# Performance work log

Hardware: AMD Instinct MI355X
Metric: run time of the kernel (lower is better)

Reference implementation:

```python
import jax, jax.numpy as jnp
import numpy as np

NUM_USERS = 100000
NUM_ITEMS = 50000
NUM_NODES = NUM_USERS + NUM_ITEMS
EMB = 64
NUM_EDGES = 2000000
BATCH = 16384


def setup_inputs() -> dict:
    key = jax.random.key(0)
    ks = jax.random.split(key, 9)

    def xavier(k, shape):
        fan_in, fan_out = shape[-2], shape[-1]
        lim = float(np.sqrt(6.0 / (fan_in + fan_out)))
        return jax.random.uniform(k, shape, jnp.float32, -lim, lim)

    user_table = xavier(ks[0], (NUM_USERS, EMB))
    item_table = xavier(ks[1], (NUM_ITEMS, EMB))
    # gat1: in=64, heads=4, out=64 -> W1 [64, 256]; a1 [4, 128]
    W1 = xavier(ks[2], (EMB, EMB * 4))
    a1 = xavier(ks[3], (4, 2 * EMB))
    # gat2: in=256, heads=1, out=64 -> W2 [256, 64]; a2 [1, 128]
    W2 = xavier(ks[4], (EMB * 4, EMB))
    a2 = xavier(ks[5], (1, 2 * EMB))

    edge_index = jax.random.randint(ks[6], (2, NUM_EDGES), 0, NUM_NODES, dtype=jnp.int32)
    user_ids = jax.random.randint(ks[7], (BATCH,), 0, NUM_USERS, dtype=jnp.int32)
    item_ids = jax.random.randint(ks[8], (BATCH,), 0, NUM_ITEMS, dtype=jnp.int32)
    return {
        "user_table": user_table, "item_table": item_table,
        "W1": W1, "a1": a1, "W2": W2, "a2": a2,
        "edge_index": edge_index, "user_ids": user_ids, "item_ids": item_ids,
    }


def gat_layer(x, W, a, num_heads, out_features, src, dst, concat):
    n = x.shape[0]
    h = (x @ W).reshape(n, num_heads, out_features)          # [N,H,F]
    # attention score: (cat(h_src,h_dst) * a).sum(-1) == h_src.a_l + h_dst.a_r
    a_l, a_r = a[:, :out_features], a[:, out_features:]
    e_src = jnp.einsum('nhf,hf->nh', h, a_l)                 # [N,H]
    e_dst = jnp.einsum('nhf,hf->nh', h, a_r)
    att = e_src[src] + e_dst[dst]                            # [E,H]
    att = jnp.where(att > 0, att, 0.2 * att)                 # LeakyReLU(0.2)
    att = jnp.exp(att - jnp.max(att))                        # global max, as in torch code
    att_sum = jax.ops.segment_sum(att, dst, num_segments=n)  # [N,H]
    att = att / (att_sum[dst] + 1e-8)
    msg = att[:, :, None] * h[src]                           # [E,H,F]
    out = jax.ops.segment_sum(msg, dst, num_segments=n)      # [N,H,F]
    return out.reshape(n, -1) if concat else out.mean(axis=1)


def reference(user_table, item_table, W1, a1, W2, a2, edge_index, user_ids, item_ids):
    src, dst = edge_index[0], edge_index[1]
    all_emb = jnp.concatenate([user_table, item_table], axis=0)  # [N,64]
    h = gat_layer(all_emb, W1, a1, 4, EMB, src, dst, concat=True)  # [N,256]
    h = jax.nn.elu(h)
    h = gat_layer(h, W2, a2, 1, EMB, src, dst, concat=False)       # [N,64]
    h = h + all_emb
    user_emb = h[:NUM_USERS]
    item_emb = h[NUM_USERS:]
    return jnp.sum(user_emb[user_ids] * item_emb[item_ids], axis=1)
```

## Files before the change

kernel.cpp:

```cpp
#include <hip/hip_runtime.h>
#include <cstdint>
#include <cstddef>

#define NUM_USERS 100000
#define NUM_ITEMS 50000
#define NUM_NODES 150000
#define NUM_EDGES 2000000
#define BATCH 16384
#define BSHIFT 8
#define NBUCK ((NUM_NODES + 255) >> BSHIFT)
#define PA_EDGES 8192
#define PA_BLOCKS ((NUM_EDGES + PA_EDGES - 1) / PA_EDGES)
#define NNPAD 150016
#define TBLK (NNPAD / 64)

typedef _Float16 hf8 __attribute__((ext_vector_type(8)));
typedef _Float16 hf4 __attribute__((ext_vector_type(4)));
typedef float fx4 __attribute__((ext_vector_type(4)));

__global__ void flag_kernel(const int* __restrict__ uid, const int* __restrict__ iid,
                            int* __restrict__ nodelist, int* __restrict__ bcnt) {
  int i = blockIdx.x * blockDim.x + threadIdx.x;
  if (i < NBUCK) bcnt[i] = 0;
  if (i < BATCH) {
    nodelist[2 * i] = uid[i];
    nodelist[2 * i + 1] = NUM_USERS + iid[i];
  }
}

__global__ __launch_bounds__(256) void bhist_kernel(const int* __restrict__ dst,
                                                    int* __restrict__ bcnt) {
  __shared__ int bh[NBUCK];
  int t = threadIdx.x;
  for (int u = t; u < NBUCK; u += 256) bh[u] = 0;
  __syncthreads();
  int base = blockIdx.x * PA_EDGES;
#pragma unroll
  for (int u = 0; u < PA_EDGES / 256; ++u) {
    int e = base + u * 256 + t;
    if (e < NUM_EDGES) atomicAdd(&bh[dst[e] >> BSHIFT], 1);
  }
  __syncthreads();
  for (int u = t; u < NBUCK; u += 256) {
    int v = bh[u];
    if (v) atomicAdd(&bcnt[u], v);
  }
}

__global__ void bscan_kernel(const int* __restrict__ bcnt, int* __restrict__ bbase,
                             int* __restrict__ bcursor, int* __restrict__ offsets) {
  __shared__ int sh[1024];
  int t = threadIdx.x;
  int v = (t < NBUCK) ? bcnt[t] : 0;
  sh[t] = v;
  __syncthreads();
  for (int off = 1; off < 1024; off <<= 1) {
    int x = (t >= off) ? sh[t - off] : 0;
    __syncthreads();
    sh[t] += x;
    __syncthreads();
  }
  if (t < NBUCK) {
    bbase[t] = sh[t] - v;
    bcursor[t] = sh[t] - v;
  }
  if (t == NBUCK - 1) {
    bbase[NBUCK] = sh[t];
    offsets[NUM_NODES] = sh[t];
  }
}

__global__ __launch_bounds__(256) void bpart_kernel(const int* __restrict__ src,
                                                    const int* __restrict__ dst,
                                                    int* __restrict__ bcursor,
                                                    int2* __restrict__ ebuf) {
  __shared__ int lcnt[NBUCK];
  __shared__ int lbase[NBUCK];
  int t = threadIdx.x;
  for (int u = t; u < NBUCK; u += 256) lcnt[u] = 0;
  __syncthreads();
  int base = blockIdx.x * PA_EDGES;
#pragma unroll
  for (int u = 0; u < PA_EDGES / 256; ++u) {
    int e = base + u * 256 + t;
    if (e < NUM_EDGES) atomicAdd(&lcnt[dst[e] >> BSHIFT], 1);
  }
  __syncthreads();
  for (int u = t; u < NBUCK; u += 256) {
    int v = lcnt[u];
    lbase[u] = v ? atomicAdd(&bcursor[u], v) : 0;
    lcnt[u] = 0;
  }
  __syncthreads();
#pragma unroll
  for (int u = 0; u < PA_EDGES / 256; ++u) {
    int e = base + u * 256 + t;
    if (e < NUM_EDGES) {
      int d = dst[e];
      int b = d >> BSHIFT;
      int p = lbase[b] + atomicAdd(&lcnt[b], 1);
      ebuf[p] = make_int2(src[e], d);
    }
  }
}

__global__ __launch_bounds__(256) void bcsr_kernel(const int2* __restrict__ ebuf,
                                                   const int* __restrict__ bbase,
                                                   int* __restrict__ offsets,
                                                   int* __restrict__ srcs) {
  __shared__ int ncnt[256];
  __shared__ int sh[256];
  __shared__ int lcur[256];
  int b = blockIdx.x;
  int t = threadIdx.x;
  int node0 = b << BSHIFT;
  int ebeg = bbase[b], eend = bbase[b + 1];
  ncnt[t] = 0;
  __syncthreads();
  for (int i = ebeg + t; i < eend; i += 256)
    atomicAdd(&ncnt[ebuf[i].y - node0], 1);
  __syncthreads();
  int v = ncnt[t];
  sh[t] = v;
  __syncthreads();
  for (int off = 1; off < 256; off <<= 1) {
    int x = (t >= off) ? sh[t - off] : 0;
    __syncthreads();
    sh[t] += x;
    __syncthreads();
  }
  int excl = ebeg + sh[t] - v;
  if (node0 + t < NUM_NODES) offsets[node0 + t] = excl;
  lcur[t] = excl;
  __syncthreads();
  for (int i = ebeg + t; i < eend; i += 256) {
    int2 ed = ebuf[i];
    int p = atomicAdd(&lcur[ed.y - node0], 1);
    srcs[p] = ed.x;
  }
}

__global__ void proj1_kernel(const float* __restrict__ W1, const float* __restrict__ a1,
                             float* __restrict__ w1a, float* __restrict__ w1b) {
  int t = threadIdx.x;
  int h = t >> 6, k = t & 63;
  float sa = 0.f, sb = 0.f;
  for (int f = 0; f < 64; ++f) {
    float w = W1[(size_t)k * 256 + h * 64 + f];
    sa += w * a1[h * 128 + f];
    sb += w * a1[h * 128 + 64 + f];
  }
  w1a[h * 64 + k] = sa;
  w1b[h * 64 + k] = sb;
}

__global__ __launch_bounds__(256) void e1_kernel(
    const float* __restrict__ ut, const float* __restrict__ it,
    const float* __restrict__ w1a, const float* __restrict__ w1b,
    float* __restrict__ e1s, float* __restrict__ e1d) {
  int wid = threadIdx.x >> 6, lane = threadIdx.x & 63;
  int node = blockIdx.x * 4 + wid;
  if (node >= NUM_NODES) return;
  const float* x = (node < NUM_USERS) ? ut + (size_t)node * 64
                                      : it + (size_t)(node - NUM_USERS) * 64;
  float xv = x[lane];
#pragma unroll
  for (int h = 0; h < 4; ++h) {
    float ps = xv * w1a[h * 64 + lane];
    float pd = xv * w1b[h * 64 + lane];
#pragma unroll
    for (int off = 32; off; off >>= 1) {
      ps += __shfl_xor(ps, off, 64);
      pd += __shfl_xor(pd, off, 64);
    }
    if (lane == 0) {
      e1s[(size_t)node * 4 + h] = ps;
      e1d[(size_t)node * 4 + h] = pd;
    }
  }
}

__device__ __forceinline__ const float* row_ptr(int s, const float* __restrict__ ut,
                                                const float* __restrict__ it) {
  return (s < NUM_USERS) ? ut + (size_t)s * 64 : it + (size_t)(s - NUM_USERS) * 64;
}

__device__ __forceinline__ float lrexp(float x) {
  x = x > 0.f ? x : 0.2f * x;
  return __expf(x);
}

__device__ __forceinline__ float wnorm(float w) {
  float sum = w;
#pragma unroll
  for (int off = 32; off; off >>= 1) sum += __shfl_xor(sum, off, 64);
  return w * (1.f / (sum + 1e-8f));
}

__device__ __forceinline__ void fold4(float4& a) {
#pragma unroll
  for (int off = 16; off <= 32; off <<= 1) {
    a.x += __shfl_xor(a.x, off, 64);
    a.y += __shfl_xor(a.y, off, 64);
    a.z += __shfl_xor(a.z, off, 64);
    a.w += __shfl_xor(a.w, off, 64);
  }
}

__device__ __forceinline__ float elu(float x) {
  return x > 0.f ? x : (__expf(x) - 1.f);
}

__device__ __forceinline__ void split4(float4 o, hf4& hv, hf4& lv) {
  float a0 = o.x * 256.f, a1 = o.y * 256.f, a2 = o.z * 256.f, a3 = o.w * 256.f;
  _Float16 h0 = (_Float16)a0, h1 = (_Float16)a1;
  _Float16 h2 = (_Float16)a2, h3 = (_Float16)a3;
  hv[0] = h0; hv[1] = h1; hv[2] = h2; hv[3] = h3;
  lv[0] = (_Float16)(a0 - (float)h0);
  lv[1] = (_Float16)(a1 - (float)h1);
  lv[2] = (_Float16)(a2 - (float)h2);
  lv[3] = (_Float16)(a3 - (float)h3);
}

__device__ __forceinline__ void splitstore(_Float16* __restrict__ hi,
                                           _Float16* __restrict__ lo,
                                           size_t idx, float v) {
  v *= 256.f;
  _Float16 h = (_Float16)v;
  hi[idx] = h;
  lo[idx] = (_Float16)(v - (float)h);
}

__global__ __launch_bounds__(256) void aggX4_kernel(
    const int* __restrict__ offsets, const int* __restrict__ srcs,
    const float* __restrict__ e1s, const float* __restrict__ e1d,
    const float* __restrict__ ut, const float* __restrict__ it,
    _Float16* __restrict__ aXhi, _Float16* __restrict__ aXlo) {
  int wid = threadIdx.x >> 6, lane = threadIdx.x & 63;
  int node = blockIdx.x * 4 + wid;
  if (node >= NNPAD) return;
  if (node >= NUM_NODES) {
    *(float2*)(aXhi + (size_t)node * 256 + lane * 4) = make_float2(0.f, 0.f);
    *(float2*)(aXlo + (size_t)node * 256 + lane * 4) = make_float2(0.f, 0.f);
    return;
  }
  int beg = offsets[node], end = offsets[node + 1];
  int deg = end - beg;

  float edv0 = e1d[(size_t)node * 4 + 0];
  float edv1 = e1d[(size_t)node * 4 + 1];
  float edv2 = e1d[(size_t)node * 4 + 2];
  float edv3 = e1d[(size_t)node * 4 + 3];

  if (deg <= 64) {
    int s = 0;
    float w0 = 0.f, w1 = 0.f, w2 = 0.f, w3 = 0.f;
    if (lane < deg) {
      s = srcs[beg + lane];
      float4 ev = *(const float4*)(e1s + (size_t)s * 4);
      w0 = lrexp(ev.x + edv0);
      w1 = lrexp(ev.y + edv1);
      w2 = lrexp(ev.z + edv2);
      w3 = lrexp(ev.w + edv3);
    }
    w0 = wnorm(w0);
    w1 = wnorm(w1);
    w2 = wnorm(w2);
    w3 = wnorm(w3);

    const int g = lane >> 4, fl = lane & 15;
    float4 acc0 = make_float4(0.f, 0.f, 0.f, 0.f);
    float4 acc1 = acc0, acc2 = acc0, acc3 = acc0;
#pragma unroll 4
    for (int e = 0; e < deg; e += 4) {
      int ei = e + g;
      int sg = __shfl(s, ei, 64);
      float4 xv = *(const float4*)(row_ptr(sg, ut, it) + fl * 4);
      float wg0 = __shfl(w0, ei, 64);
      acc0.x += wg0 * xv.x; acc0.y += wg0 * xv.y;
      acc0.z += wg0 * xv.z; acc0.w += wg0 * xv.w;
      float wg1 = __shfl(w1, ei, 64);
      acc1.x += wg1 * xv.x; acc1.y += wg1 * xv.y;
      acc1.z += wg1 * xv.z; acc1.w += wg1 * xv.w;
      float wg2 = __shfl(w2, ei, 64);
      acc2.x += wg2 * xv.x; acc2.y += wg2 * xv.y;
      acc2.z += wg2 * xv.z; acc2.w += wg2 * xv.w;
      float wg3 = __shfl(w3, ei, 64);
      acc3.x += wg3 * xv.x; acc3.y += wg3 * xv.y;
      acc3.z += wg3 * xv.z; acc3.w += wg3 * xv.w;
    }
    fold4(acc0); fold4(acc1); fold4(acc2); fold4(acc3);

    float4 o = (g == 0) ? acc0 : (g == 1) ? acc1 : (g == 2) ? acc2 : acc3;
    hf4 hv, lv;
    split4(o, hv, lv);
    *(hf4*)(aXhi + (size_t)node * 256 + lane * 4) = hv;
    *(hf4*)(aXlo + (size_t)node * 256 + lane * 4) = lv;
  } else {
    float s0 = 0.f, s1 = 0.f, s2 = 0.f, s3 = 0.f;
    for (int e = beg + lane; e < end; e += 64) {
      int s = srcs[e];
      float4 ev = *(const float4*)(e1s + (size_t)s * 4);
      s0 += lrexp(ev.x + edv0); s1 += lrexp(ev.y + edv1);
      s2 += lrexp(ev.z + edv2); s3 += lrexp(ev.w + edv3);
    }
#pragma unroll
    for (int off = 32; off; off >>= 1) {
      s0 += __shfl_xor(s0, off, 64);
      s1 += __shfl_xor(s1, off, 64);
      s2 += __shfl_xor(s2, off, 64);
      s3 += __shfl_xor(s3, off, 64);
    }
    float i0 = 1.f / (s0 + 1e-8f), i1 = 1.f / (s1 + 1e-8f);
    float i2 = 1.f / (s2 + 1e-8f), i3 = 1.f / (s3 + 1e-8f);
    float a0 = 0.f, a1 = 0.f, a2 = 0.f, a3 = 0.f;
    for (int e = beg; e < end; ++e) {
      int sn = srcs[e];
      float xv = row_ptr(sn, ut, it)[lane];
      float4 ev = *(const float4*)(e1s + (size_t)sn * 4);
      a0 += lrexp(ev.x + edv0) * i0 * xv;
      a1 += lrexp(ev.y + edv1) * i1 * xv;
      a2 += lrexp(ev.z + edv2) * i2 * xv;
      a3 += lrexp(ev.w + edv3) * i3 * xv;
    }
    splitstore(aXhi, aXlo, (size_t)node * 256 + 0 * 64 + lane, a0);
    splitstore(aXhi, aXlo, (size_t)node * 256 + 1 * 64 + lane, a1);
    splitstore(aXhi, aXlo, (size_t)node * 256 + 2 * 64 + lane, a2);
    splitstore(aXhi, aXlo, (size_t)node * 256 + 3 * 64 + lane, a3);
  }
}

__global__ void wprep_kernel(const float* __restrict__ W1, const float* __restrict__ W2,
                             _Float16* __restrict__ w1t_hi, _Float16* __restrict__ w1t_lo,
                             _Float16* __restrict__ w2t_hi, _Float16* __restrict__ w2t_lo) {
  int t = threadIdx.x;
  int h = t >> 6, a = t & 63;
  for (int k = 0; k < 64; ++k) {
    float w = W1[(size_t)k * 256 + h * 64 + a] * 256.f;
    _Float16 hi = (_Float16)w;
    w1t_hi[(size_t)(h * 64 + a) * 64 + k] = hi;
    w1t_lo[(size_t)(h * 64 + a) * 64 + k] = (_Float16)(w - (float)hi);

    float v = W2[(size_t)(h * 64 + k) * 64 + a] * 256.f;
    _Float16 hi2 = (_Float16)v;
    w2t_hi[(size_t)(h * 64 + a) * 64 + k] = hi2;
    w2t_lo[(size_t)(h * 64 + a) * 64 + k] = (_Float16)(v - (float)hi2);
  }
}

__device__ __forceinline__ fx4 mfma3(fx4 c, hf8 ah, hf8 al, hf8 bh, hf8 bl) {
  c = __builtin_amdgcn_mfma_f32_16x16x32_f16(ah, bh, c, 0, 0, 0);
  c = __builtin_amdgcn_mfma_f32_16x16x32_f16(al, bh, c, 0, 0, 0);
  c = __builtin_amdgcn_mfma_f32_16x16x32_f16(ah, bl, c, 0, 0, 0);
  return c;
}

__global__ __launch_bounds__(64, 2) void trans_mfma_kernel(
    const _Float16* __restrict__ aXhi, const _Float16* __restrict__ aXlo,
    const _Float16* __restrict__ w1t_hi, const _Float16* __restrict__ w1t_lo,
    const _Float16* __restrict__ w2t_hi, const _Float16* __restrict__ w2t_lo,
    const float* __restrict__ a2v,
    float* __restrict__ h2g, float* __restrict__ e2s, float* __restrict__ e2d) {
  __shared__ __align__(16) _Float16 t1hi[64 * 64];
  __shared__ __align__(16) _Float16 t1lo[64 * 64];
  const int l = threadIdx.x;
  const int lr = l & 15, lg = l >> 4;
  const int node0 = blockIdx.x * 64;
  const float DS = 1.52587890625e-05f;

  fx4 acc2[4][4];
#pragma unroll
  for (int m = 0; m < 4; ++m)
#pragma unroll
    for (int n = 0; n < 4; ++n) acc2[m][n] = (fx4){0.f, 0.f, 0.f, 0.f};

#pragma unroll 1
  for (int h = 0; h < 4; ++h) {
    fx4 acc1[4][4];
#pragma unroll
    for (int m = 0; m < 4; ++m)
#pragma unroll
      for (int n = 0; n < 4; ++n) acc1[m][n] = (fx4){0.f, 0.f, 0.f, 0.f};

#pragma unroll
    for (int ks = 0; ks < 2; ++ks) {
      const int ko = ks * 32 + lg * 8;
      hf8 wah[4], wal[4], xbh[4], xbl[4];
#pragma unroll
      for (int m = 0; m < 4; ++m) {
        size_t wo = (size_t)((h * 64 + m * 16 + lr) * 64 + ko);
        wah[m] = *(const hf8*)(w1t_hi + wo);
        wal[m] = *(const hf8*)(w1t_lo + wo);
      }
#pragma unroll
      for (int n = 0; n < 4; ++n) {
        size_t xo = (size_t)(node0 + n * 16 + lr) * 256 + h * 64 + ko;
        xbh[n] = *(const hf8*)(aXhi + xo);
        xbl[n] = *(const hf8*)(aXlo + xo);
      }
#pragma unroll
      for (int m = 0; m < 4; ++m)
#pragma unroll
        for (int n = 0; n < 4; ++n)
          acc1[m][n] = mfma3(acc1[m][n], wah[m], wal[m], xbh[n], xbl[n]);
    }

#pragma unroll
    for (int m = 0; m < 4; ++m)
#pragma unroll
      for (int n = 0; n < 4; ++n) {
        hf4 hv, lv;
#pragma unroll
        for (int r = 0; r < 4; ++r) {
          float v = acc1[m][n][r] * DS;
          v = elu(v) * 256.f;
          _Float16 hi = (_Float16)v;
          hv[r] = hi;
          lv[r] = (_Float16)(v - (float)hi);
        }
        int nl = n * 16 + lr;
        int ro = (m * 32 + lg * 8) ^ ((nl & 7) << 4);
        *(hf4*)((char*)t1hi + nl * 128 + ro) = hv;
        *(hf4*)((char*)t1lo + nl * 128 + ro) = lv;
      }

#pragma unroll
    for (int ks = 0; ks < 2; ++ks) {
      const int ko = ks * 32 + lg * 8;
      hf8 wah[4], wal[4], tbh[4], tbl[4];
#pragma unroll
      for (int m = 0; m < 4; ++m) {
        size_t wo = (size_t)((h * 64 + m * 16 + lr) * 64 + ko);
        wah[m] = *(const hf8*)(w2t_hi + wo);
        wal[m] = *(const hf8*)(w2t_lo + wo);
      }
#pragma unroll
      for (int n = 0; n < 4; ++n) {
        int nl = n * 16 + lr;
        int ro = (ks * 64 + lg * 16) ^ ((nl & 7) << 4);
        tbh[n] = *(const hf8*)((char*)t1hi + nl * 128 + ro);
        tbl[n] = *(const hf8*)((char*)t1lo + nl * 128 + ro);
      }
#pragma unroll
      for (int m = 0; m < 4; ++m)
#pragma unroll
        for (int n = 0; n < 4; ++n)
          acc2[m][n] = mfma3(acc2[m][n], wah[m], wal[m], tbh[n], tbl[n]);
    }
  }

  float ps[4] = {0.f, 0.f, 0.f, 0.f};
  float pd[4] = {0.f, 0.f, 0.f, 0.f};
#pragma unroll
  for (int m = 0; m < 4; ++m) {
    fx4 al = *(const fx4*)(a2v + m * 16 + lg * 4);
    fx4 ar = *(const fx4*)(a2v + 64 + m * 16 + lg * 4);
#pragma unroll
    for (int n = 0; n < 4; ++n) {
      fx4 v = acc2[m][n] * DS;
      int node = node0 + n * 16 + lr;
      if (node < NUM_NODES)
        *(fx4*)(h2g + (size_t)node * 64 + m * 16 + lg * 4) = v;
      ps[n] += v[0] * al[0] + v[1] * al[1] + v[2] * al[2] + v[3] * al[3];
      pd[n] += v[0] * ar[0] + v[1] * ar[1] + v[2] * ar[2] + v[3] * ar[3];
    }
  }
#pragma unroll
  for (int n = 0; n < 4; ++n) {
    float s = ps[n], d = pd[n];
    s += __shfl_xor(s, 16, 64);
    s += __shfl_xor(s, 32, 64);
    d += __shfl_xor(d, 16, 64);
    d += __shfl_xor(d, 32, 64);
    int node = node0 + n * 16 + lr;
    if (lg == n && node < NUM_NODES) {
      e2s[node] = s;
      e2d[node] = d;
    }
  }
}

__global__ __launch_bounds__(256) void agg2_kernel(
    const int* __restrict__ offsets, const int* __restrict__ srcs,
    const float* __restrict__ e2s, const float* __restrict__ e2d,
    const int* __restrict__ nodelist, const float* __restrict__ h2,
    const float* __restrict__ ut, const float* __restrict__ it,
    float* __restrict__ hfin) {
  int wid = threadIdx.x >> 6, lane = threadIdx.x & 63;
  int idx = blockIdx.x * 4 + wid;
  if (idx >= 2 * BATCH) return;
  int node = nodelist[idx];
  int beg = offsets[node], end = offsets[node + 1];
  int deg = end - beg;
  float edv = e2d[node];

  if (deg <= 64) {
    int s = 0;
    float w = 0.f;
    if (lane < deg) {
      s = srcs[beg + lane];
      w = lrexp(e2s[s] + edv);
    }
    w = wnorm(w);

    const int g = lane >> 4, fl = lane & 15;
    float4 acc = make_float4(0.f, 0.f, 0.f, 0.f);
#pragma unroll 4
    for (int e = 0; e < deg; e += 4) {
      int ei = e + g;
      int sg = __shfl(s, ei, 64);
      float wg = __shfl(w, ei, 64);
      float4 hv = *(const float4*)(h2 + (size_t)sg * 64 + fl * 4);
      acc.x += wg * hv.x; acc.y += wg * hv.y; acc.z += wg * hv.z; acc.w += wg * hv.w;
    }
    fold4(acc);
    if (g == 0) {
      const float* rp = (node < NUM_USERS) ? ut + (size_t)node * 64
                                           : it + (size_t)(node - NUM_USERS) * 64;
      float4 res = *(const float4*)(rp + fl * 4);
      acc.x += res.x; acc.y += res.y; acc.z += res.z; acc.w += res.w;
      *(float4*)(hfin + (size_t)node * 64 + fl * 4) = acc;
    }
  } else {
    float psum = 0.f;
    for (int e = beg + lane; e < end; e += 64) {
      int s = srcs[e];
      psum += lrexp(e2s[s] + edv);
    }
#pragma unroll
    for (int off = 32; off; off >>= 1) psum += __shfl_xor(psum, off, 64);
    float inv = 1.f / (psum + 1e-8f);
    float acc = 0.f;
    for (int e = beg; e < end; ++e) {
      int s0 = srcs[e];
      acc += lrexp(e2s[s0] + edv) * inv * h2[(size_t)s0 * 64 + lane];
    }
    float res = (node < NUM_USERS) ? ut[(size_t)node * 64 + lane]
                                   : it[(size_t)(node - NUM_USERS) * 64 + lane];
    hfin[(size_t)node * 64 + lane] = acc + res;
  }
}

__global__ __launch_bounds__(256) void final_kernel(
    const float* __restrict__ hf, const int* __restrict__ uid,
    const int* __restrict__ iid, float* __restrict__ out) {
  int wid = threadIdx.x >> 6, lane = threadIdx.x & 63;
  int idx = blockIdx.x * 4 + wid;
  if (idx >= BATCH) return;
  int u = uid[idx], v = iid[idx];
  float a = hf[(size_t)u * 64 + lane];
  float b = hf[(size_t)(NUM_USERS + v) * 64 + lane];
  float p = a * b;
#pragma unroll
  for (int off = 32; off; off >>= 1) p += __shfl_xor(p, off, 64);
  if (lane == 0) out[idx] = p;
}

extern "C" void kernel_launch(void* const* d_in, const int* in_sizes, int n_in,
                              void* d_out, int out_size, void* d_ws, size_t ws_size,
                              hipStream_t stream) {
  const float* user_table = (const float*)d_in[0];
  const float* item_table = (const float*)d_in[1];
  const float* W1 = (const float*)d_in[2];
  const float* a1 = (const float*)d_in[3];
  const float* W2 = (const float*)d_in[4];
  const float* a2 = (const float*)d_in[5];
  const int* edge_index = (const int*)d_in[6];
  const int* user_ids = (const int*)d_in[7];
  const int* item_ids = (const int*)d_in[8];
  float* out = (float*)d_out;

  const int* src = edge_index;
  const int* dst = edge_index + NUM_EDGES;

  float* ws = (float*)d_ws;
  size_t off = 0;
  auto falloc = [&](size_t n) { float* p = ws + off; off += n; return p; };
  float* h2  = falloc((size_t)NUM_NODES * 64);
  float* e1s = falloc((size_t)NUM_NODES * 4);
  float* e1d = falloc((size_t)NUM_NODES * 4);
  float* e2s = falloc(NUM_NODES);
  float* e2d = falloc(NUM_NODES);
  float* w1a = falloc(256);
  float* w1b = falloc(256);
  int* offsets  = (int*)falloc(NUM_NODES + 1);
  int* srcs     = (int*)falloc(NUM_EDGES);
  int* nodelist = (int*)falloc(2 * BATCH);
  int* bcnt     = (int*)falloc(NBUCK);
  int* bbase    = (int*)falloc(NBUCK + 1);
  int* bcursor  = (int*)falloc(NBUCK);
  off = (off + 3) & ~(size_t)3;
  _Float16* aggXhi = (_Float16*)(ws + off); off += (size_t)NNPAD * 128;
  _Float16* aggXlo = (_Float16*)(ws + off); off += (size_t)NNPAD * 128;

  int2* ebuf = (int2*)aggXhi;
  float* hfin = (float*)aggXhi;
  _Float16* w1t_hi = (_Float16*)e1s;
  _Float16* w1t_lo = w1t_hi + 4 * 64 * 64;
  _Float16* w2t_hi = w1t_lo + 4 * 64 * 64;
  _Float16* w2t_lo = w2t_hi + 4 * 64 * 64;

  const int nb4 = (NUM_NODES + 3) / 4;

  flag_kernel<<<(BATCH + 255) / 256, 256, 0, stream>>>(user_ids, item_ids,
                                                       nodelist, bcnt);
  bhist_kernel<<<PA_BLOCKS, 256, 0, stream>>>(dst, bcnt);
  bscan_kernel<<<1, 1024, 0, stream>>>(bcnt, bbase, bcursor, offsets);
  bpart_kernel<<<PA_BLOCKS, 256, 0, stream>>>(src, dst, bcursor, ebuf);
  bcsr_kernel<<<NBUCK, 256, 0, stream>>>(ebuf, bbase, offsets, srcs);

  proj1_kernel<<<1, 256, 0, stream>>>(W1, a1, w1a, w1b);
  e1_kernel<<<nb4, 256, 0, stream>>>(user_table, item_table, w1a, w1b, e1s, e1d);

  aggX4_kernel<<<NNPAD / 4, 256, 0, stream>>>(offsets, srcs, e1s, e1d,
                                              user_table, item_table,
                                              aggXhi, aggXlo);
  wprep_kernel<<<1, 256, 0, stream>>>(W1, W2, w1t_hi, w1t_lo, w2t_hi, w2t_lo);
  trans_mfma_kernel<<<TBLK, 64, 0, stream>>>(aggXhi, aggXlo,
                                             w1t_hi, w1t_lo, w2t_hi, w2t_lo,
                                             a2, h2, e2s, e2d);

  agg2_kernel<<<(2 * BATCH + 3) / 4, 256, 0, stream>>>(offsets, srcs, e2s, e2d,
                                                       nodelist, h2,
                                                       user_table, item_table, hfin);
  final_kernel<<<(BATCH + 3) / 4, 256, 0, stream>>>(hfin, user_ids, item_ids, out);
}
```

Baseline: 526.7 us.

## Bin nodes by degree and aggregate low-degree nodes with quarter-wave groups

Adds a degree-classification pass that builds separate lists of nodes with at most 16 in-edges and the rest. Low-degree nodes are aggregated by 16-lane groups, four nodes per wave, with edge weights staged in shared memory. Higher-degree nodes keep the original one-wave-per-node path. The e1 score kernel is also reworked to handle four nodes per wave with float4 loads. The aim is to stop idling most lanes of a 64-wide wave on nodes whose average degree is about 13, at the cost of an extra kernel, global atomics and list indirection.

```diff
diff --git a/kernel.cpp b/kernel.cpp
--- a/kernel.cpp
+++ b/kernel.cpp
@@ -19,9 +19,11 @@
 typedef float fx4 __attribute__((ext_vector_type(4)));
 
 __global__ void flag_kernel(const int* __restrict__ uid, const int* __restrict__ iid,
-                            int* __restrict__ nodelist, int* __restrict__ bcnt) {
+                            int* __restrict__ nodelist, int* __restrict__ bcnt,
+                            int* __restrict__ gcnt) {
   int i = blockIdx.x * blockDim.x + threadIdx.x;
   if (i < NBUCK) bcnt[i] = 0;
+  if (i < 2) gcnt[i] = 0;
   if (i < BATCH) {
     nodelist[2 * i] = uid[i];
     nodelist[2 * i + 1] = NUM_USERS + iid[i];
@@ -140,6 +142,38 @@
   }
 }
 
+__global__ __launch_bounds__(256) void dlist_kernel(
+    const int* __restrict__ offsets, int* __restrict__ gcnt,
+    int* __restrict__ Ls, int* __restrict__ Lm,
+    _Float16* __restrict__ aXhi, _Float16* __restrict__ aXlo) {
+  __shared__ int c0, c1, b0, b1;
+  int t = threadIdx.x;
+  int n = blockIdx.x * 256 + t;
+  if (t == 0) { c0 = 0; c1 = 0; }
+  __syncthreads();
+  int cls = -1, rank = 0;
+  if (n < NUM_NODES) {
+    int deg = offsets[n + 1] - offsets[n];
+    cls = (deg <= 16) ? 0 : 1;
+    rank = atomicAdd(cls == 0 ? &c0 : &c1, 1);
+  } else if (n < NNPAD) {
+    float4 z = make_float4(0.f, 0.f, 0.f, 0.f);
+#pragma unroll
+    for (int i = 0; i < 32; ++i) {
+      ((float4*)(aXhi + (size_t)n * 256))[i] = z;
+      ((float4*)(aXlo + (size_t)n * 256))[i] = z;
+    }
+  }
+  __syncthreads();
+  if (t == 0) {
+    b0 = atomicAdd(&gcnt[0], c0);
+    b1 = atomicAdd(&gcnt[1], c1);
+  }
+  __syncthreads();
+  if (cls == 0) Ls[b0 + rank] = n;
+  else if (cls == 1) Lm[b1 + rank] = n;
+}
+
 __global__ void proj1_kernel(const float* __restrict__ W1, const float* __restrict__ a1,
                              float* __restrict__ w1a, float* __restrict__ w1b) {
   int t = threadIdx.x;
@@ -154,32 +188,6 @@
   w1b[h * 64 + k] = sb;
 }
 
-__global__ __launch_bounds__(256) void e1_kernel(
-    const float* __restrict__ ut, const float* __restrict__ it,
-    const float* __restrict__ w1a, const float* __restrict__ w1b,
-    float* __restrict__ e1s, float* __restrict__ e1d) {
-  int wid = threadIdx.x >> 6, lane = threadIdx.x & 63;
-  int node = blockIdx.x * 4 + wid;
-  if (node >= NUM_NODES) return;
-  const float* x = (node < NUM_USERS) ? ut + (size_t)node * 64
-                                      : it + (size_t)(node - NUM_USERS) * 64;
-  float xv = x[lane];
-#pragma unroll
-  for (int h = 0; h < 4; ++h) {
-    float ps = xv * w1a[h * 64 + lane];
-    float pd = xv * w1b[h * 64 + lane];
-#pragma unroll
-    for (int off = 32; off; off >>= 1) {
-      ps += __shfl_xor(ps, off, 64);
-      pd += __shfl_xor(pd, off, 64);
-    }
-    if (lane == 0) {
-      e1s[(size_t)node * 4 + h] = ps;
-      e1d[(size_t)node * 4 + h] = pd;
-    }
-  }
-}
-
 __device__ __forceinline__ const float* row_ptr(int s, const float* __restrict__ ut,
                                                 const float* __restrict__ it) {
   return (s < NUM_USERS) ? ut + (size_t)s * 64 : it + (size_t)(s - NUM_USERS) * 64;
@@ -231,19 +239,129 @@
   lo[idx] = (_Float16)(v - (float)h);
 }
 
-__global__ __launch_bounds__(256) void aggX4_kernel(
+__global__ __launch_bounds__(256) void e1g_kernel(
+    const float* __restrict__ ut, const float* __restrict__ it,
+    const float* __restrict__ w1a, const float* __restrict__ w1b,
+    float* __restrict__ e1s, float* __restrict__ e1d) {
+  int t = threadIdx.x;
+  int wave = t >> 6, lane = t & 63;
+  int g = lane >> 4, fl = lane & 15;
+  int node = blockIdx.x * 16 + wave * 4 + g;
+  bool valid = node < NUM_NODES;
+  float4 xv = make_float4(0.f, 0.f, 0.f, 0.f);
+  if (valid) xv = *(const float4*)(row_ptr(node, ut, it) + fl * 4);
+  float ps[4], pd[4];
+#pragma unroll
+  for (int h = 0; h < 4; ++h) {
+    float4 wa = *(const float4*)(w1a + h * 64 + fl * 4);
+    float4 wb = *(const float4*)(w1b + h * 64 + fl * 4);
+    ps[h] = xv.x * wa.x + xv.y * wa.y + xv.z * wa.z + xv.w * wa.w;
+    pd[h] = xv.x * wb.x + xv.y * wb.y + xv.z * wb.z + xv.w * wb.w;
+  }
+#pragma unroll
+  for (int off = 8; off; off >>= 1) {
+#pragma unroll
+    for (int h = 0; h < 4; ++h) {
+      ps[h] += __shfl_xor(ps[h], off, 16);
+      pd[h] += __shfl_xor(pd[h], off, 16);
+    }
+  }
+  if (valid && fl == 0) {
+    *(float4*)(e1s + (size_t)node * 4) = make_float4(ps[0], ps[1], ps[2], ps[3]);
+    *(float4*)(e1d + (size_t)node * 4) = make_float4(pd[0], pd[1], pd[2], pd[3]);
+  }
+}
+
+__global__ __launch_bounds__(256) void aggXs_kernel(
+    const int* __restrict__ Ls, const int* __restrict__ gcnt,
+    const int* __restrict__ offsets, const int* __restrict__ srcs,
+    const float* __restrict__ e1s, const float* __restrict__ e1d,
+    const float* __restrict__ ut, const float* __restrict__ it,
+    _Float16* __restrict__ aXhi, _Float16* __restrict__ aXlo) {
+  __shared__ int sS[4][68];
+  __shared__ __align__(16) float4 sW[4][68];
+  const int t = threadIdx.x;
+  const int wave = t >> 6, lane = t & 63;
+  const int g = lane >> 4, fl = lane & 15;
+  const int cnt = gcnt[0];
+  const int widx = blockIdx.x * 16 + wave * 4 + g;
+  const int node = (widx < cnt) ? Ls[widx] : -1;
+
+  int beg = 0, deg = 0;
+  float4 ed = make_float4(0.f, 0.f, 0.f, 0.f);
+  if (node >= 0) {
+    beg = offsets[node];
+    deg = offsets[node + 1] - beg;
+    ed = *(const float4*)(e1d + (size_t)node * 4);
+  }
+  int s = 0;
+  float w0 = 0.f, w1 = 0.f, w2 = 0.f, w3 = 0.f;
+  if (fl < deg) {
+    s = srcs[beg + fl];
+    float4 ev = *(const float4*)(e1s + (size_t)s * 4);
+    w0 = lrexp(ev.x + ed.x);
+    w1 = lrexp(ev.y + ed.y);
+    w2 = lrexp(ev.z + ed.z);
+    w3 = lrexp(ev.w + ed.w);
+  }
+  float t0 = w0, t1 = w1, t2 = w2, t3 = w3;
+#pragma unroll
+  for (int off = 8; off; off >>= 1) {
+    t0 += __shfl_xor(t0, off, 16);
+    t1 += __shfl_xor(t1, off, 16);
+    t2 += __shfl_xor(t2, off, 16);
+    t3 += __shfl_xor(t3, off, 16);
+  }
+  w0 *= 1.f / (t0 + 1e-8f);
+  w1 *= 1.f / (t1 + 1e-8f);
+  w2 *= 1.f / (t2 + 1e-8f);
+  w3 *= 1.f / (t3 + 1e-8f);
+  sS[wave][g * 17 + fl] = s;
+  sW[wave][g * 17 + fl] = make_float4(w0, w1, w2, w3);
+
+  int md = deg;
+  md = max(md, __shfl_xor(md, 16, 64));
+  md = max(md, __shfl_xor(md, 32, 64));
+
+  float4 a0 = make_float4(0.f, 0.f, 0.f, 0.f);
+  float4 a1 = a0, a2 = a0, a3 = a0;
+#pragma unroll 2
+  for (int e = 0; e < md; ++e) {
+    int se = sS[wave][g * 17 + e];
+    float4 w4 = sW[wave][g * 17 + e];
+    float4 xv = *(const float4*)(row_ptr(se, ut, it) + fl * 4);
+    a0.x += w4.x * xv.x; a0.y += w4.x * xv.y; a0.z += w4.x * xv.z; a0.w += w4.x * xv.w;
+    a1.x += w4.y * xv.x; a1.y += w4.y * xv.y; a1.z += w4.y * xv.z; a1.w += w4.y * xv.w;
+    a2.x += w4.z * xv.x; a2.y += w4.z * xv.y; a2.z += w4.z * xv.z; a2.w += w4.z * xv.w;
+    a3.x += w4.w * xv.x; a3.y += w4.w * xv.y; a3.z += w4.w * xv.z; a3.w += w4.w * xv.w;
+  }
+  if (node >= 0) {
+    hf4 hv, lv;
+    split4(a0, hv, lv);
+    *(hf4*)(aXhi + (size_t)node * 256 + 0 * 64 + fl * 4) = hv;
+    *(hf4*)(aXlo + (size_t)node * 256 + 0 * 64 + fl * 4) = lv;
+    split4(a1, hv, lv);
+    *(hf4*)(aXhi + (size_t)node * 256 + 1 * 64 + fl * 4) = hv;
+    *(hf4*)(aXlo + (size_t)node * 256 + 1 * 64 + fl * 4) = lv;
+    split4(a2, hv, lv);
+    *(hf4*)(aXhi + (size_t)node * 256 + 2 * 64 + fl * 4) = hv;
+    *(hf4*)(aXlo + (size_t)node * 256 + 2 * 64 + fl * 4) = lv;
+    split4(a3, hv, lv);
+    *(hf4*)(aXhi + (size_t)node * 256 + 3 * 64 + fl * 4) = hv;
+    *(hf4*)(aXlo + (size_t)node * 256 + 3 * 64 + fl * 4) = lv;
+  }
+}
+
+__global__ __launch_bounds__(256) void aggXm_kernel(
+    const int* __restrict__ Lm, const int* __restrict__ gcnt,
     const int* __restrict__ offsets, const int* __restrict__ srcs,
     const float* __restrict__ e1s, const float* __restrict__ e1d,
     const float* __restrict__ ut, const float* __restrict__ it,
     _Float16* __restrict__ aXhi, _Float16* __restrict__ aXlo) {
   int wid = threadIdx.x >> 6, lane = threadIdx.x & 63;
-  int node = blockIdx.x * 4 + wid;
-  if (node >= NNPAD) return;
-  if (node >= NUM_NODES) {
-    *(float2*)(aXhi + (size_t)node * 256 + lane * 4) = make_float2(0.f, 0.f);
-    *(float2*)(aXlo + (size_t)node * 256 + lane * 4) = make_float2(0.f, 0.f);
-    return;
-  }
+  int idx = blockIdx.x * 4 + wid;
+  if (idx >= gcnt[1]) return;
+  int node = Lm[idx];
   int beg = offsets[node], end = offsets[node + 1];
   int deg = end - beg;
 
@@ -589,32 +707,39 @@
   int* bcnt     = (int*)falloc(NBUCK);
   int* bbase    = (int*)falloc(NBUCK + 1);
   int* bcursor  = (int*)falloc(NBUCK);
+  int* gcnt     = (int*)falloc(2);
+  int* Ls       = (int*)falloc(NNPAD);
+  int* Lm       = (int*)falloc(NNPAD);
   off = (off + 3) & ~(size_t)3;
   _Float16* aggXhi = (_Float16*)(ws + off); off += (size_t)NNPAD * 128;
   _Float16* aggXlo = (_Float16*)(ws + off); off += (size_t)NNPAD * 128;
 
   int2* ebuf = (int2*)aggXhi;
   float* hfin = (float*)aggXhi;
-  _Float16* w1t_hi = (_Float16*)e1s;
-  _Float16* w1t_lo = w1t_hi + 4 * 64 * 64;
-  _Float16* w2t_hi = w1t_lo + 4 * 64 * 64;
-  _Float16* w2t_lo = w2t_hi + 4 * 64 * 64;
-
-  const int nb4 = (NUM_NODES + 3) / 4;
+  _Float16* w1t_hi = (_Float16*)falloc(4 * 64 * 64 / 2 + 16);
+  _Float16* w1t_lo = (_Float16*)falloc(4 * 64 * 64 / 2 + 16);
+  _Float16* w2t_hi = (_Float16*)falloc(4 * 64 * 64 / 2 + 16);
+  _Float16* w2t_lo = (_Float16*)falloc(4 * 64 * 64 / 2 + 16);
 
   flag_kernel<<<(BATCH + 255) / 256, 256, 0, stream>>>(user_ids, item_ids,
-                                                       nodelist, bcnt);
+                                                       nodelist, bcnt, gcnt);
   bhist_kernel<<<PA_BLOCKS, 256, 0, stream>>>(dst, bcnt);
   bscan_kernel<<<1, 1024, 0, stream>>>(bcnt, bbase, bcursor, offsets);
   bpart_kernel<<<PA_BLOCKS, 256, 0, stream>>>(src, dst, bcursor, ebuf);
   bcsr_kernel<<<NBUCK, 256, 0, stream>>>(ebuf, bbase, offsets, srcs);
+  dlist_kernel<<<(NNPAD + 255) / 256, 256, 0, stream>>>(offsets, gcnt, Ls, Lm,
+                                                        aggXhi, aggXlo);
 
   proj1_kernel<<<1, 256, 0, stream>>>(W1, a1, w1a, w1b);
-  e1_kernel<<<nb4, 256, 0, stream>>>(user_table, item_table, w1a, w1b, e1s, e1d);
-
-  aggX4_kernel<<<NNPAD / 4, 256, 0, stream>>>(offsets, srcs, e1s, e1d,
-                                              user_table, item_table,
-                                              aggXhi, aggXlo);
+  e1g_kernel<<<(NNPAD + 15) / 16, 256, 0, stream>>>(user_table, item_table,
+                                                    w1a, w1b, e1s, e1d);
+
+  aggXs_kernel<<<(NNPAD + 15) / 16, 256, 0, stream>>>(Ls, gcnt, offsets, srcs,
+                                                      e1s, e1d, user_table,
+                                                      item_table, aggXhi, aggXlo);
+  aggXm_kernel<<<(NNPAD + 3) / 4, 256, 0, stream>>>(Lm, gcnt, offsets, srcs,
+                                                    e1s, e1d, user_table,
+                                                    item_table, aggXhi, aggXlo);
   wprep_kernel<<<1, 256, 0, stream>>>(W1, W2, w1t_hi, w1t_lo, w2t_hi, w2t_lo);
   trans_mfma_kernel<<<TBLK, 64, 0, stream>>>(aggXhi, aggXlo,
                                              w1t_hi, w1t_lo, w2t_hi, w2t_lo,
```

Result: faster. 499.4 us (-5.2%).
